# Kernel optimization log

Hardware: AMD Instinct MI355X
Metric: run time of the kernel (lower is better)

## Reference

```python
import jax, jax.numpy as jnp
import numpy as np

B, S, D, E, H = 4, 4096, 1024, 8, 128  # batch, seq, d_model, experts, expert hidden (hardcoded 128)


def setup_inputs() -> dict:
    key = jax.random.key(0)
    ks = jax.random.split(key, 7)
    s_in = 1.0 / np.sqrt(D)
    s_h = 1.0 / np.sqrt(H)
    return {
        "x": jax.random.normal(ks[0], (B, S, D), dtype=jnp.float32),
        "W1": jax.random.normal(ks[1], (E, D, H), dtype=jnp.float32) * s_in,
        "b1": jax.random.normal(ks[2], (E, H), dtype=jnp.float32) * s_in,
        "W2": jax.random.normal(ks[3], (E, H, D), dtype=jnp.float32) * s_h,
        "b2": jax.random.normal(ks[4], (E, D), dtype=jnp.float32) * s_h,
        "Wg": jax.random.normal(ks[5], (D, E), dtype=jnp.float32) * s_in,
        "bg": jax.random.normal(ks[6], (E,), dtype=jnp.float32) * s_in,
    }


def reference(x, W1, b1, W2, b2, Wg, bg):
    # Gate: softmax over experts. [B,S,E]
    gate = jax.nn.softmax(jnp.einsum("bsd,de->bse", x, Wg) + bg, axis=-1)
    # Dense per-expert MLP applied to every token.
    h = jax.nn.relu(jnp.einsum("bsd,edh->bseh", x, W1) + b1)          # [B,S,E,H]
    y = jnp.einsum("bseh,eho->bseo", h, W2) + b2                       # [B,S,E,D]
    # Fused weighted sum over the expert axis (replaces the python double loop).
    out = jnp.einsum("bse,bseo->bso", gate, y)                         # [B,S,D]
    return out
```

## Files before the change

### kernel.cpp

```cpp
#include <hip/hip_runtime.h>
#include <hip/hip_bf16.h>

#define B_ 4
#define S_ 4096
#define D_ 1024
#define E_ 8
#define H_ 128
#define M_ (B_*S_)
#define K_ 1024
#define N_ 1024
#define NT_ (K_/64)
#define NIT_ (NT_/2)

typedef short bf16x8 __attribute__((ext_vector_type(8)));
typedef float f32x4 __attribute__((ext_vector_type(4)));

__device__ __forceinline__ unsigned short f2bf(float f){
  union { float f; unsigned int u; } v; v.f = f;
  unsigned int u = v.u;
  unsigned int r = (u + 0x7fffu + ((u >> 16) & 1u)) >> 16;
  return (unsigned short)r;
}

__device__ __forceinline__ void gload16(const void* g, void* l){
  __builtin_amdgcn_global_load_lds((const __attribute__((address_space(1))) void*)g,
                                   (__attribute__((address_space(3))) void*)l, 16, 0, 0);
}

__global__ __launch_bounds__(256)
void prep_x_gate(const float* __restrict__ x, const float* __restrict__ Wg,
                 const float* __restrict__ bg, unsigned short* __restrict__ xb,
                 float* __restrict__ gate){
  int tid = threadIdx.x;
  int lane = tid & 63;
  int m = blockIdx.x * 4 + (tid >> 6);
  const float* xr = x + (size_t)m * D_;
  unsigned short* xbr = xb + (size_t)m * D_;
  float acc[E_];
  #pragma unroll
  for (int e = 0; e < E_; ++e) acc[e] = 0.f;
  #pragma unroll
  for (int c = 0; c < D_/64; ++c){
    int d = c*64 + lane;
    float xs = xr[d];
    xbr[d] = f2bf(xs);
    const float4 w0 = *(const float4*)(Wg + (size_t)d * E_);
    const float4 w1 = *(const float4*)(Wg + (size_t)d * E_ + 4);
    acc[0] = fmaf(xs, w0.x, acc[0]); acc[1] = fmaf(xs, w0.y, acc[1]);
    acc[2] = fmaf(xs, w0.z, acc[2]); acc[3] = fmaf(xs, w0.w, acc[3]);
    acc[4] = fmaf(xs, w1.x, acc[4]); acc[5] = fmaf(xs, w1.y, acc[5]);
    acc[6] = fmaf(xs, w1.z, acc[6]); acc[7] = fmaf(xs, w1.w, acc[7]);
  }
  #pragma unroll
  for (int off = 32; off > 0; off >>= 1){
    #pragma unroll
    for (int e = 0; e < E_; ++e) acc[e] += __shfl_xor(acc[e], off, 64);
  }
  float lg[E_]; float mx = -1e30f;
  #pragma unroll
  for (int e = 0; e < E_; ++e){ lg[e] = acc[e] + bg[e]; mx = fmaxf(mx, lg[e]); }
  float s = 0.f;
  #pragma unroll
  for (int e = 0; e < E_; ++e){ lg[e] = expf(lg[e] - mx); s += lg[e]; }
  float inv = 1.f / s;
  if (lane < E_) gate[(size_t)m * E_ + lane] = lg[lane] * inv;
}

__global__ __launch_bounds__(256)
void transpose_pack(const float* __restrict__ in, unsigned short* __restrict__ out,
                    int C, int ostride, int in_estride, int out_ebase){
  __shared__ float t[32][33];
  int e = blockIdx.z;
  const float* ip = in + (size_t)e * in_estride;
  unsigned short* op = out + (size_t)e * out_ebase;
  int tx = threadIdx.x, ty = threadIdx.y;
  int c0 = blockIdx.x * 32, r0 = blockIdx.y * 32;
  #pragma unroll
  for (int yy = 0; yy < 32; yy += 8)
    t[ty + yy][tx] = ip[(size_t)(r0 + ty + yy) * C + (c0 + tx)];
  __syncthreads();
  #pragma unroll
  for (int yy = 0; yy < 32; yy += 8)
    op[(size_t)(c0 + ty + yy) * ostride + (r0 + tx)] = f2bf(t[tx][ty + yy]);
}

template<int PASS>
__global__ __launch_bounds__(512, 2)
void gemm_moe8(const unsigned short* __restrict__ A,
               const unsigned short* __restrict__ Bt,
               const float* __restrict__ gate,
               const float* __restrict__ bias,
               void* __restrict__ outp)
{
  __shared__ unsigned short lds[65536];

  int bid = blockIdx.x;
  int xcd = bid & 7, pos = bid >> 3;
  int mb = xcd * 8 + (pos >> 2);
  int nb = pos & 3;
  int m0 = mb * 256, n0 = nb * 256;

  int tid = threadIdx.x;
  int lane = tid & 63;
  int w = tid >> 6;
  int wm = w & 1, wn = w >> 1;
  int rowi = lane & 15, s4 = lane >> 4;

  int sg = (tid & 7) ^ ((tid >> 3) & 7);
  const unsigned short* gA = A  + (size_t)(m0 + (tid >> 3)) * K_ + sg * 8;
  const unsigned short* gB = Bt + (size_t)(n0 + (tid >> 3)) * K_ + sg * 8;
  int t8 = tid * 8;

#define STAGE_A(b,h,kt) do{ const unsigned short* g_ = gA + (size_t)((h)*128)*K_ + (kt)*64; \
  gload16(g_,                 &lds[(b)*16384 + (h)*8192 + t8]); \
  gload16(g_ + (size_t)64*K_, &lds[(b)*16384 + (h)*8192 + t8 + 4096]); }while(0)
#define STAGE_B(b,h,kt) do{ const unsigned short* g_ = gB + (size_t)((h)*128)*K_ + (kt)*64; \
  gload16(g_,                 &lds[32768 + (b)*16384 + (h)*8192 + t8]); \
  gload16(g_ + (size_t)64*K_, &lds[32768 + (b)*16384 + (h)*8192 + t8 + 4096]); }while(0)

  int bk0 = rowi*64 + (( s4     ) ^ (rowi & 7)) * 8;
  int bk1 = rowi*64 + ((4 + s4  ) ^ (rowi & 7)) * 8;
  int abase0 = wm * 8192;
  int bbase0 = 32768 + (wn >> 1) * 8192 + (wn & 1) * 4096;

  f32x4 acc[8][4];
  #pragma unroll
  for (int i = 0; i < 8; ++i){
    #pragma unroll
    for (int j = 0; j < 4; ++j){ f32x4 z = {0.f,0.f,0.f,0.f}; acc[i][j] = z; }
  }
  bf16x8 af[4][2], bfr[4][2];

#define READ_A(b,r) do{ int ab_ = (b)*16384 + abase0; \
  _Pragma("unroll") for (int f2 = 0; f2 < 4; ++f2){ \
    af[f2][0] = *(const bf16x8*)&lds[ab_ + ((r)*4+f2)*1024 + bk0]; \
    af[f2][1] = *(const bf16x8*)&lds[ab_ + ((r)*4+f2)*1024 + bk1]; } }while(0)
#define READ_B(b,c) do{ int bb_ = (b)*16384 + bbase0; \
  _Pragma("unroll") for (int j2 = 0; j2 < 2; ++j2){ \
    bfr[(c)*2+j2][0] = *(const bf16x8*)&lds[bb_ + ((c)*2+j2)*1024 + bk0]; \
    bfr[(c)*2+j2][1] = *(const bf16x8*)&lds[bb_ + ((c)*2+j2)*1024 + bk1]; } }while(0)
#define MFMA16(r,c) do{ \
  _Pragma("unroll") for (int f2 = 0; f2 < 4; ++f2) \
  _Pragma("unroll") for (int j2 = 0; j2 < 2; ++j2){ \
    acc[(r)*4+f2][(c)*2+j2] = __builtin_amdgcn_mfma_f32_16x16x32_bf16(af[f2][0], bfr[(c)*2+j2][0], acc[(r)*4+f2][(c)*2+j2], 0,0,0); \
    acc[(r)*4+f2][(c)*2+j2] = __builtin_amdgcn_mfma_f32_16x16x32_bf16(af[f2][1], bfr[(c)*2+j2][1], acc[(r)*4+f2][(c)*2+j2], 0,0,0); \
  } }while(0)

#define PH_MID  __builtin_amdgcn_s_barrier(); \
                asm volatile("s_waitcnt lgkmcnt(0)" ::: "memory"); \
                __builtin_amdgcn_s_setprio(1)
#define PH_END  __builtin_amdgcn_s_setprio(0); __builtin_amdgcn_s_barrier()
#define PH_END_VM(N) __builtin_amdgcn_s_setprio(0); \
                asm volatile("s_waitcnt vmcnt(" #N ")" ::: "memory"); \
                __builtin_amdgcn_s_barrier()

  STAGE_B(0,0,0); STAGE_B(0,1,0);
  STAGE_A(0,0,0); STAGE_A(0,1,0);
  STAGE_B(1,0,1); STAGE_B(1,1,1);
  STAGE_A(1,0,1);
  asm volatile("s_waitcnt vmcnt(6)" ::: "memory");
  __builtin_amdgcn_s_barrier();

  #pragma unroll 1
  for (int it = 0; it < NIT_; ++it){
    int kt1  = 2*it + 1;
    int ktn0 = 2*it + 2, ktn1 = 2*it + 3;
    bool more = (it < NIT_ - 1);
    READ_A(0,0); READ_B(0,0);
    STAGE_A(1,1,kt1);
    PH_MID; MFMA16(0,0); PH_END;
    READ_B(0,1);
    PH_MID; MFMA16(0,1); PH_END;
    READ_A(0,1);
    if (more) STAGE_B(0,0,ktn0);
    PH_MID; MFMA16(1,1); PH_END;
    if (more) STAGE_B(0,1,ktn0);
    PH_MID; MFMA16(1,0);
    __builtin_amdgcn_s_setprio(0);
    if (more) { asm volatile("s_waitcnt vmcnt(4)" ::: "memory"); }
    else      { asm volatile("s_waitcnt vmcnt(0)" ::: "memory"); }
    __builtin_amdgcn_s_barrier();
    READ_A(1,0); READ_B(1,0);
    if (more) STAGE_A(0,0,ktn0);
    PH_MID; MFMA16(0,0); PH_END;
    READ_B(1,1);
    if (more) STAGE_A(0,1,ktn0);
    PH_MID; MFMA16(0,1); PH_END;
    READ_A(1,1);
    if (more) STAGE_B(1,0,ktn1);
    PH_MID; MFMA16(1,1); PH_END;
    if (more){ STAGE_B(1,1,ktn1); STAGE_A(1,0,ktn1); }
    PH_MID; MFMA16(1,0); PH_END_VM(6);
  }

  float* lws = (float*)lds + w * 4096;
  int ncol0 = n0 + wn*64;

  if (PASS == 1){
    unsigned short* Hp = (unsigned short*)outp;
    int e = nb*2 + (wn >> 1);
    float b1v[4];
    #pragma unroll
    for (int j = 0; j < 4; ++j) b1v[j] = bias[e*H_ + (wn&1)*64 + j*16 + rowi];
    #pragma unroll
    for (int ci = 0; ci < 2; ++ci){
      #pragma unroll
      for (int f2 = 0; f2 < 4; ++f2){
        int fi = ci*4 + f2;
        #pragma unroll
        for (int jj = 0; jj < 4; ++jj){
          int m = m0 + wm*128 + fi*16 + s4*4 + jj;
          float g = gate[(size_t)m*E_ + e];
          int r_l = f2*16 + s4*4 + jj;
          #pragma unroll
          for (int j = 0; j < 4; ++j){
            float v = fmaxf(acc[fi][j][jj] + b1v[j], 0.f) * g;
            lws[r_l*64 + ((j*16 + rowi) ^ (s4 << 4))] = v;
          }
        }
      }
      asm volatile("s_waitcnt lgkmcnt(0)" ::: "memory");
      #pragma unroll
      for (int it2 = 0; it2 < 16; ++it2){
        int r_l = it2*4 + (lane >> 4);
        int c4  = lane & 15;
        int X   = it2 & 3;
        f32x4 v = *(const f32x4*)&lws[r_l*64 + ((c4*4) ^ (X << 4))];
        union { unsigned short us[4]; uint2 u2; } pk;
        #pragma unroll
        for (int q = 0; q < 4; ++q) pk.us[q] = f2bf(v[q]);
        int m = m0 + wm*128 + ci*64 + r_l;
        *(uint2*)&Hp[(size_t)m*N_ + ncol0 + c4*4] = pk.u2;
      }
      if (ci == 0) asm volatile("s_waitcnt lgkmcnt(0)" ::: "memory");
    }
  } else {
    float* Out = (float*)outp;
    float b2v[8][4];
    #pragma unroll
    for (int j = 0; j < 4; ++j){
      int n = ncol0 + j*16 + rowi;
      #pragma unroll
      for (int e = 0; e < 8; ++e) b2v[e][j] = bias[(size_t)e*N_ + n];
    }
    #pragma unroll
    for (int ci = 0; ci < 2; ++ci){
      #pragma unroll
      for (int f2 = 0; f2 < 4; ++f2){
        int fi = ci*4 + f2;
        #pragma unroll
        for (int jj = 0; jj < 4; ++jj){
          int m = m0 + wm*128 + fi*16 + s4*4 + jj;
          const float4 g0 = *(const float4*)(gate + (size_t)m*E_);
          const float4 g1 = *(const float4*)(gate + (size_t)m*E_ + 4);
          int r_l = f2*16 + s4*4 + jj;
          #pragma unroll
          for (int j = 0; j < 4; ++j){
            float bv = g0.x*b2v[0][j] + g0.y*b2v[1][j] + g0.z*b2v[2][j] + g0.w*b2v[3][j]
                     + g1.x*b2v[4][j] + g1.y*b2v[5][j] + g1.z*b2v[6][j] + g1.w*b2v[7][j];
            lws[r_l*64 + ((j*16 + rowi) ^ (s4 << 4))] = acc[fi][j][jj] + bv;
          }
        }
      }
      asm volatile("s_waitcnt lgkmcnt(0)" ::: "memory");
      #pragma unroll
      for (int it2 = 0; it2 < 16; ++it2){
        int r_l = it2*4 + (lane >> 4);
        int c4  = lane & 15;
        int X   = it2 & 3;
        f32x4 v = *(const f32x4*)&lws[r_l*64 + ((c4*4) ^ (X << 4))];
        int m = m0 + wm*128 + ci*64 + r_l;
        *(f32x4*)&Out[(size_t)m*N_ + ncol0 + c4*4] = v;
      }
      if (ci == 0) asm volatile("s_waitcnt lgkmcnt(0)" ::: "memory");
    }
  }
#undef STAGE_A
#undef STAGE_B
#undef READ_A
#undef READ_B
#undef MFMA16
#undef PH_MID
#undef PH_END
#undef PH_END_VM
}

extern "C" void kernel_launch(void* const* d_in, const int* in_sizes, int n_in,
                              void* d_out, int out_size, void* d_ws, size_t ws_size,
                              hipStream_t stream){
  const float* x  = (const float*)d_in[0];
  const float* W1 = (const float*)d_in[1];
  const float* b1 = (const float*)d_in[2];
  const float* W2 = (const float*)d_in[3];
  const float* b2 = (const float*)d_in[4];
  const float* Wg = (const float*)d_in[5];
  const float* bg = (const float*)d_in[6];
  float* out = (float*)d_out;

  char* ws = (char*)d_ws;
  unsigned short* xb  = (unsigned short*)(ws);
  unsigned short* Hp  = (unsigned short*)(ws + ((size_t)32<<20));
  unsigned short* B1T = (unsigned short*)(ws + ((size_t)64<<20));
  unsigned short* B2T = (unsigned short*)(ws + ((size_t)66<<20));
  float*          gate= (float*)(ws + ((size_t)68<<20));

  hipLaunchKernelGGL(prep_x_gate, dim3(M_/4), dim3(256), 0, stream, x, Wg, bg, xb, gate);
  hipLaunchKernelGGL(transpose_pack, dim3(128/32, 1024/32, 8), dim3(32,8), 0, stream,
                     W1, B1T, 128, 1024, 1024*128, 128*1024);
  hipLaunchKernelGGL(transpose_pack, dim3(1024/32, 128/32, 8), dim3(32,8), 0, stream,
                     W2, B2T, 1024, 1024, 128*1024, 128);
  hipLaunchKernelGGL((gemm_moe8<1>), dim3(256), dim3(512), 0, stream,
                     xb, B1T, gate, b1, (void*)Hp);
  hipLaunchKernelGGL((gemm_moe8<2>), dim3(256), dim3(512), 0, stream,
                     Hp, B2T, gate, b2, (void*)out);
}
```

Measured before the change: 107.4 us.

## Fuse fp32-to-bf16 conversion of x into first GEMM and store output directly

The first GEMM now loads fp32 x straight from global memory into registers, converts it to bf16 and writes it into swizzled LDS, with the load and wait schedule interleaved into the existing pipeline. This removes the separate bf16 copy of x written by the prep kernel and the extra global round trip that copy needed. The second GEMM epilogue skips the LDS transpose and writes fp32 output directly from the accumulators, which gives less coalesced stores. The cost is more registers and VALU work inside the GEMM main loop, plus a more fragile vmcnt schedule.

Measured after the change: 130.1 us. 1.21x slower.

```diff
diff --git a/kernel.cpp b/kernel.cpp
--- a/kernel.cpp
+++ b/kernel.cpp
@@ -28,14 +28,12 @@
 }
 
 __global__ __launch_bounds__(256)
-void prep_x_gate(const float* __restrict__ x, const float* __restrict__ Wg,
-                 const float* __restrict__ bg, unsigned short* __restrict__ xb,
-                 float* __restrict__ gate){
+void prep_gate(const float* __restrict__ x, const float* __restrict__ Wg,
+               const float* __restrict__ bg, float* __restrict__ gate){
   int tid = threadIdx.x;
   int lane = tid & 63;
   int m = blockIdx.x * 4 + (tid >> 6);
   const float* xr = x + (size_t)m * D_;
-  unsigned short* xbr = xb + (size_t)m * D_;
   float acc[E_];
   #pragma unroll
   for (int e = 0; e < E_; ++e) acc[e] = 0.f;
@@ -43,7 +41,6 @@
   for (int c = 0; c < D_/64; ++c){
     int d = c*64 + lane;
     float xs = xr[d];
-    xbr[d] = f2bf(xs);
     const float4 w0 = *(const float4*)(Wg + (size_t)d * E_);
     const float4 w1 = *(const float4*)(Wg + (size_t)d * E_ + 4);
     acc[0] = fmaf(xs, w0.x, acc[0]); acc[1] = fmaf(xs, w0.y, acc[1]);
@@ -83,53 +80,6 @@
   for (int yy = 0; yy < 32; yy += 8)
     op[(size_t)(c0 + ty + yy) * ostride + (r0 + tx)] = f2bf(t[tx][ty + yy]);
 }
-
-template<int PASS>
-__global__ __launch_bounds__(512, 2)
-void gemm_moe8(const unsigned short* __restrict__ A,
-               const unsigned short* __restrict__ Bt,
-               const float* __restrict__ gate,
-               const float* __restrict__ bias,
-               void* __restrict__ outp)
-{
-  __shared__ unsigned short lds[65536];
-
-  int bid = blockIdx.x;
-  int xcd = bid & 7, pos = bid >> 3;
-  int mb = xcd * 8 + (pos >> 2);
-  int nb = pos & 3;
-  int m0 = mb * 256, n0 = nb * 256;
-
-  int tid = threadIdx.x;
-  int lane = tid & 63;
-  int w = tid >> 6;
-  int wm = w & 1, wn = w >> 1;
-  int rowi = lane & 15, s4 = lane >> 4;
-
-  int sg = (tid & 7) ^ ((tid >> 3) & 7);
-  const unsigned short* gA = A  + (size_t)(m0 + (tid >> 3)) * K_ + sg * 8;
-  const unsigned short* gB = Bt + (size_t)(n0 + (tid >> 3)) * K_ + sg * 8;
-  int t8 = tid * 8;
-
-#define STAGE_A(b,h,kt) do{ const unsigned short* g_ = gA + (size_t)((h)*128)*K_ + (kt)*64; \
-  gload16(g_,                 &lds[(b)*16384 + (h)*8192 + t8]); \
-  gload16(g_ + (size_t)64*K_, &lds[(b)*16384 + (h)*8192 + t8 + 4096]); }while(0)
-#define STAGE_B(b,h,kt) do{ const unsigned short* g_ = gB + (size_t)((h)*128)*K_ + (kt)*64; \
-  gload16(g_,                 &lds[32768 + (b)*16384 + (h)*8192 + t8]); \
-  gload16(g_ + (size_t)64*K_, &lds[32768 + (b)*16384 + (h)*8192 + t8 + 4096]); }while(0)
-
-  int bk0 = rowi*64 + (( s4     ) ^ (rowi & 7)) * 8;
-  int bk1 = rowi*64 + ((4 + s4  ) ^ (rowi & 7)) * 8;
-  int abase0 = wm * 8192;
-  int bbase0 = 32768 + (wn >> 1) * 8192 + (wn & 1) * 4096;
-
-  f32x4 acc[8][4];
-  #pragma unroll
-  for (int i = 0; i < 8; ++i){
-    #pragma unroll
-    for (int j = 0; j < 4; ++j){ f32x4 z = {0.f,0.f,0.f,0.f}; acc[i][j] = z; }
-  }
-  bf16x8 af[4][2], bfr[4][2];
 
 #define READ_A(b,r) do{ int ab_ = (b)*16384 + abase0; \
   _Pragma("unroll") for (int f2 = 0; f2 < 4; ++f2){ \
@@ -145,7 +95,6 @@
     acc[(r)*4+f2][(c)*2+j2] = __builtin_amdgcn_mfma_f32_16x16x32_bf16(af[f2][0], bfr[(c)*2+j2][0], acc[(r)*4+f2][(c)*2+j2], 0,0,0); \
     acc[(r)*4+f2][(c)*2+j2] = __builtin_amdgcn_mfma_f32_16x16x32_bf16(af[f2][1], bfr[(c)*2+j2][1], acc[(r)*4+f2][(c)*2+j2], 0,0,0); \
   } }while(0)
-
 #define PH_MID  __builtin_amdgcn_s_barrier(); \
                 asm volatile("s_waitcnt lgkmcnt(0)" ::: "memory"); \
                 __builtin_amdgcn_s_setprio(1)
@@ -153,11 +102,208 @@
 #define PH_END_VM(N) __builtin_amdgcn_s_setprio(0); \
                 asm volatile("s_waitcnt vmcnt(" #N ")" ::: "memory"); \
                 __builtin_amdgcn_s_barrier()
-
-  STAGE_B(0,0,0); STAGE_B(0,1,0);
-  STAGE_A(0,0,0); STAGE_A(0,1,0);
-  STAGE_B(1,0,1); STAGE_B(1,1,1);
-  STAGE_A(1,0,1);
+#define VMW(N)  do{ asm volatile("s_waitcnt vmcnt(" #N ")" ::: "memory"); \
+                    __builtin_amdgcn_sched_barrier(0); }while(0)
+#define LA4(dst, p) do{ const float* p_ = (p); \
+  (dst)[0] = *(const float4*)(p_);      (dst)[1] = *(const float4*)(p_ + 4); \
+  (dst)[2] = *(const float4*)(p_ + 8);  (dst)[3] = *(const float4*)(p_ + 12); }while(0)
+
+__global__ __launch_bounds__(512, 2)
+void gemm_pass1(const float* __restrict__ X,
+                const unsigned short* __restrict__ Bt,
+                const float* __restrict__ gate,
+                const float* __restrict__ bias,
+                unsigned short* __restrict__ Hp)
+{
+  __shared__ unsigned short lds[65536];
+
+  int bid = blockIdx.x;
+  int xcd = bid & 7, pos = bid >> 3;
+  int mb = xcd * 8 + (pos >> 2);
+  int nb = pos & 3;
+  int m0 = mb * 256, n0 = nb * 256;
+
+  int tid = threadIdx.x;
+  int lane = tid & 63;
+  int w = tid >> 6;
+  int wm = w & 1, wn = w >> 1;
+  int rowi = lane & 15, s4 = lane >> 4;
+
+  int sg = (tid & 7) ^ ((tid >> 3) & 7);
+  const unsigned short* gB = Bt + (size_t)(n0 + (tid >> 3)) * K_ + sg * 8;
+  int t8 = tid * 8;
+#define SB(b,h,kt) do{ const unsigned short* g_ = gB + (size_t)((h)*128)*K_ + (kt)*64; \
+  gload16(g_,                 &lds[32768 + (b)*16384 + (h)*8192 + t8]); \
+  gload16(g_ + (size_t)64*K_, &lds[32768 + (b)*16384 + (h)*8192 + t8 + 4096]); }while(0)
+
+  int wr_  = tid >> 2;
+  int ws0_ = (2*(tid & 3))     ^ (wr_ & 7);
+  int ws1_ = (2*(tid & 3) + 1) ^ (wr_ & 7);
+  const float* gxA = X + (size_t)(m0 + wr_) * K_ + (tid & 3) * 16;
+#define PA(h,kt) (gxA + (size_t)((h)*128)*K_ + (kt)*64)
+#define WA_(b,h,la) do{ \
+  union { unsigned short us[8]; bf16x8 v; } p0_, p1_; \
+  p0_.us[0]=f2bf((la)[0].x); p0_.us[1]=f2bf((la)[0].y); \
+  p0_.us[2]=f2bf((la)[0].z); p0_.us[3]=f2bf((la)[0].w); \
+  p0_.us[4]=f2bf((la)[1].x); p0_.us[5]=f2bf((la)[1].y); \
+  p0_.us[6]=f2bf((la)[1].z); p0_.us[7]=f2bf((la)[1].w); \
+  p1_.us[0]=f2bf((la)[2].x); p1_.us[1]=f2bf((la)[2].y); \
+  p1_.us[2]=f2bf((la)[2].z); p1_.us[3]=f2bf((la)[2].w); \
+  p1_.us[4]=f2bf((la)[3].x); p1_.us[5]=f2bf((la)[3].y); \
+  p1_.us[6]=f2bf((la)[3].z); p1_.us[7]=f2bf((la)[3].w); \
+  *(bf16x8*)&lds[(b)*16384 + (h)*8192 + wr_*64 + ws0_*8] = p0_.v; \
+  *(bf16x8*)&lds[(b)*16384 + (h)*8192 + wr_*64 + ws1_*8] = p1_.v; }while(0)
+
+  int bk0 = rowi*64 + (( s4     ) ^ (rowi & 7)) * 8;
+  int bk1 = rowi*64 + ((4 + s4  ) ^ (rowi & 7)) * 8;
+  int abase0 = wm * 8192;
+  int bbase0 = 32768 + (wn >> 1) * 8192 + (wn & 1) * 4096;
+
+  f32x4 acc[8][4];
+  #pragma unroll
+  for (int i = 0; i < 8; ++i){
+    #pragma unroll
+    for (int j = 0; j < 4; ++j){ f32x4 z = {0.f,0.f,0.f,0.f}; acc[i][j] = z; }
+  }
+  bf16x8 af[4][2], bfr[4][2];
+  float4 laA[4], laB[4];
+
+  SB(0,0,0); SB(0,1,0);
+  LA4(laA, PA(0,0));
+  LA4(laB, PA(1,0));
+  VMW(4);  WA_(0,0,laA);
+  LA4(laA, PA(0,1));
+  VMW(4);  WA_(0,1,laB);
+  SB(1,0,1);
+  VMW(2);  WA_(1,0,laA);
+  LA4(laB, PA(1,1));
+  SB(1,1,1);
+  asm volatile("s_waitcnt lgkmcnt(0)" ::: "memory");
+  __builtin_amdgcn_s_barrier();
+
+  #pragma unroll 1
+  for (int it = 0; it < NIT_; ++it){
+    int ktn0 = 2*it + 2, ktn1 = 2*it + 3;
+    bool more = (it < NIT_ - 1);
+    READ_A(0,0); READ_B(0,0);
+    VMW(2); WA_(1,1,laB);
+    PH_MID; MFMA16(0,0); PH_END;
+    READ_B(0,1);
+    PH_MID; MFMA16(0,1); PH_END;
+    READ_A(0,1);
+    if (more){ SB(0,0,ktn0); LA4(laA, PA(0,ktn0)); }
+    PH_MID; MFMA16(1,1); PH_END;
+    if (more){ SB(0,1,ktn0); LA4(laB, PA(1,ktn0)); }
+    PH_MID; MFMA16(1,0);
+    __builtin_amdgcn_s_setprio(0);
+    if (more) { VMW(12); } else { VMW(0); }
+    __builtin_amdgcn_s_barrier();
+    READ_A(1,0); READ_B(1,0);
+    if (more){ VMW(6); WA_(0,0,laA); }
+    PH_MID; MFMA16(0,0); PH_END;
+    READ_B(1,1);
+    if (more){ LA4(laA, PA(0,ktn1)); VMW(4); WA_(0,1,laB); }
+    PH_MID; MFMA16(0,1); PH_END;
+    READ_A(1,1);
+    if (more){ SB(1,0,ktn1); LA4(laB, PA(1,ktn1)); }
+    PH_MID; MFMA16(1,1); PH_END;
+    if (more){ SB(1,1,ktn1); VMW(8); WA_(1,0,laA); }
+    PH_MID; MFMA16(1,0); PH_END;
+  }
+
+  float* lws = (float*)lds + w * 4096;
+  int ncol0 = n0 + wn*64;
+  int e = nb*2 + (wn >> 1);
+  float b1v[4];
+  #pragma unroll
+  for (int j = 0; j < 4; ++j) b1v[j] = bias[e*H_ + (wn&1)*64 + j*16 + rowi];
+  #pragma unroll
+  for (int ci = 0; ci < 2; ++ci){
+    #pragma unroll
+    for (int f2 = 0; f2 < 4; ++f2){
+      int fi = ci*4 + f2;
+      #pragma unroll
+      for (int jj = 0; jj < 4; ++jj){
+        int m = m0 + wm*128 + fi*16 + s4*4 + jj;
+        float g = gate[(size_t)m*E_ + e];
+        int r_l = f2*16 + s4*4 + jj;
+        #pragma unroll
+        for (int j = 0; j < 4; ++j){
+          float v = fmaxf(acc[fi][j][jj] + b1v[j], 0.f) * g;
+          lws[r_l*64 + ((j*16 + rowi) ^ (s4 << 4))] = v;
+        }
+      }
+    }
+    asm volatile("s_waitcnt lgkmcnt(0)" ::: "memory");
+    #pragma unroll
+    for (int it2 = 0; it2 < 16; ++it2){
+      int r_l = it2*4 + (lane >> 4);
+      int c4  = lane & 15;
+      int X2  = it2 & 3;
+      f32x4 v = *(const f32x4*)&lws[r_l*64 + ((c4*4) ^ (X2 << 4))];
+      union { unsigned short us[4]; uint2 u2; } pk;
+      #pragma unroll
+      for (int q = 0; q < 4; ++q) pk.us[q] = f2bf(v[q]);
+      int m = m0 + wm*128 + ci*64 + r_l;
+      *(uint2*)&Hp[(size_t)m*N_ + ncol0 + c4*4] = pk.u2;
+    }
+    if (ci == 0) asm volatile("s_waitcnt lgkmcnt(0)" ::: "memory");
+  }
+#undef SB
+#undef PA
+#undef WA_
+}
+
+__global__ __launch_bounds__(512, 2)
+void gemm_pass2(const unsigned short* __restrict__ A,
+                const unsigned short* __restrict__ Bt,
+                const float* __restrict__ gate,
+                const float* __restrict__ bias,
+                float* __restrict__ Out)
+{
+  __shared__ unsigned short lds[65536];
+
+  int bid = blockIdx.x;
+  int xcd = bid & 7, pos = bid >> 3;
+  int mb = xcd * 8 + (pos >> 2);
+  int nb = pos & 3;
+  int m0 = mb * 256, n0 = nb * 256;
+
+  int tid = threadIdx.x;
+  int lane = tid & 63;
+  int w = tid >> 6;
+  int wm = w & 1, wn = w >> 1;
+  int rowi = lane & 15, s4 = lane >> 4;
+
+  int sg = (tid & 7) ^ ((tid >> 3) & 7);
+  const unsigned short* gA = A  + (size_t)(m0 + (tid >> 3)) * K_ + sg * 8;
+  const unsigned short* gB = Bt + (size_t)(n0 + (tid >> 3)) * K_ + sg * 8;
+  int t8 = tid * 8;
+
+#define SA2(b,h,kt) do{ const unsigned short* g_ = gA + (size_t)((h)*128)*K_ + (kt)*64; \
+  gload16(g_,                 &lds[(b)*16384 + (h)*8192 + t8]); \
+  gload16(g_ + (size_t)64*K_, &lds[(b)*16384 + (h)*8192 + t8 + 4096]); }while(0)
+#define SB2(b,h,kt) do{ const unsigned short* g_ = gB + (size_t)((h)*128)*K_ + (kt)*64; \
+  gload16(g_,                 &lds[32768 + (b)*16384 + (h)*8192 + t8]); \
+  gload16(g_ + (size_t)64*K_, &lds[32768 + (b)*16384 + (h)*8192 + t8 + 4096]); }while(0)
+
+  int bk0 = rowi*64 + (( s4     ) ^ (rowi & 7)) * 8;
+  int bk1 = rowi*64 + ((4 + s4  ) ^ (rowi & 7)) * 8;
+  int abase0 = wm * 8192;
+  int bbase0 = 32768 + (wn >> 1) * 8192 + (wn & 1) * 4096;
+
+  f32x4 acc[8][4];
+  #pragma unroll
+  for (int i = 0; i < 8; ++i){
+    #pragma unroll
+    for (int j = 0; j < 4; ++j){ f32x4 z = {0.f,0.f,0.f,0.f}; acc[i][j] = z; }
+  }
+  bf16x8 af[4][2], bfr[4][2];
+
+  SB2(0,0,0); SB2(0,1,0);
+  SA2(0,0,0); SA2(0,1,0);
+  SB2(1,0,1); SB2(1,1,1);
+  SA2(1,0,1);
   asm volatile("s_waitcnt vmcnt(6)" ::: "memory");
   __builtin_amdgcn_s_barrier();
 
@@ -167,122 +313,59 @@
     int ktn0 = 2*it + 2, ktn1 = 2*it + 3;
     bool more = (it < NIT_ - 1);
     READ_A(0,0); READ_B(0,0);
-    STAGE_A(1,1,kt1);
+    SA2(1,1,kt1);
     PH_MID; MFMA16(0,0); PH_END;
     READ_B(0,1);
     PH_MID; MFMA16(0,1); PH_END;
     READ_A(0,1);
-    if (more) STAGE_B(0,0,ktn0);
+    if (more) SB2(0,0,ktn0);
     PH_MID; MFMA16(1,1); PH_END;
-    if (more) STAGE_B(0,1,ktn0);
+    if (more) SB2(0,1,ktn0);
     PH_MID; MFMA16(1,0);
     __builtin_amdgcn_s_setprio(0);
     if (more) { asm volatile("s_waitcnt vmcnt(4)" ::: "memory"); }
     else      { asm volatile("s_waitcnt vmcnt(0)" ::: "memory"); }
     __builtin_amdgcn_s_barrier();
     READ_A(1,0); READ_B(1,0);
-    if (more) STAGE_A(0,0,ktn0);
+    if (more) SA2(0,0,ktn0);
     PH_MID; MFMA16(0,0); PH_END;
     READ_B(1,1);
-    if (more) STAGE_A(0,1,ktn0);
+    if (more) SA2(0,1,ktn0);
     PH_MID; MFMA16(0,1); PH_END;
     READ_A(1,1);
-    if (more) STAGE_B(1,0,ktn1);
+    if (more) SB2(1,0,ktn1);
     PH_MID; MFMA16(1,1); PH_END;
-    if (more){ STAGE_B(1,1,ktn1); STAGE_A(1,0,ktn1); }
+    if (more){ SB2(1,1,ktn1); SA2(1,0,ktn1); }
     PH_MID; MFMA16(1,0); PH_END_VM(6);
   }
 
-  float* lws = (float*)lds + w * 4096;
   int ncol0 = n0 + wn*64;
-
-  if (PASS == 1){
-    unsigned short* Hp = (unsigned short*)outp;
-    int e = nb*2 + (wn >> 1);
-    float b1v[4];
-    #pragma unroll
-    for (int j = 0; j < 4; ++j) b1v[j] = bias[e*H_ + (wn&1)*64 + j*16 + rowi];
-    #pragma unroll
-    for (int ci = 0; ci < 2; ++ci){
+  float b2v[8][4];
+  #pragma unroll
+  for (int j = 0; j < 4; ++j){
+    int n = ncol0 + j*16 + rowi;
+    #pragma unroll
+    for (int e = 0; e < 8; ++e) b2v[e][j] = bias[(size_t)e*N_ + n];
+  }
+  #pragma unroll
+  for (int fi = 0; fi < 8; ++fi){
+    #pragma unroll
+    for (int jj = 0; jj < 4; ++jj){
+      int m = m0 + wm*128 + fi*16 + s4*4 + jj;
+      const float4 g0 = *(const float4*)(gate + (size_t)m*E_);
+      const float4 g1 = *(const float4*)(gate + (size_t)m*E_ + 4);
+      float bv[4];
       #pragma unroll
-      for (int f2 = 0; f2 < 4; ++f2){
-        int fi = ci*4 + f2;
-        #pragma unroll
-        for (int jj = 0; jj < 4; ++jj){
-          int m = m0 + wm*128 + fi*16 + s4*4 + jj;
-          float g = gate[(size_t)m*E_ + e];
-          int r_l = f2*16 + s4*4 + jj;
-          #pragma unroll
-          for (int j = 0; j < 4; ++j){
-            float v = fmaxf(acc[fi][j][jj] + b1v[j], 0.f) * g;
-            lws[r_l*64 + ((j*16 + rowi) ^ (s4 << 4))] = v;
-          }
-        }
-      }
-      asm volatile("s_waitcnt lgkmcnt(0)" ::: "memory");
+      for (int j = 0; j < 4; ++j)
+        bv[j] = g0.x*b2v[0][j] + g0.y*b2v[1][j] + g0.z*b2v[2][j] + g0.w*b2v[3][j]
+              + g1.x*b2v[4][j] + g1.y*b2v[5][j] + g1.z*b2v[6][j] + g1.w*b2v[7][j];
       #pragma unroll
-      for (int it2 = 0; it2 < 16; ++it2){
-        int r_l = it2*4 + (lane >> 4);
-        int c4  = lane & 15;
-        int X   = it2 & 3;
-        f32x4 v = *(const f32x4*)&lws[r_l*64 + ((c4*4) ^ (X << 4))];
-        union { unsigned short us[4]; uint2 u2; } pk;
-        #pragma unroll
-        for (int q = 0; q < 4; ++q) pk.us[q] = f2bf(v[q]);
-        int m = m0 + wm*128 + ci*64 + r_l;
-        *(uint2*)&Hp[(size_t)m*N_ + ncol0 + c4*4] = pk.u2;
-      }
-      if (ci == 0) asm volatile("s_waitcnt lgkmcnt(0)" ::: "memory");
+      for (int j = 0; j < 4; ++j)
+        Out[(size_t)m*N_ + ncol0 + j*16 + rowi] = acc[fi][j][jj] + bv[j];
     }
-  } else {
-    float* Out = (float*)outp;
-    float b2v[8][4];
-    #pragma unroll
-    for (int j = 0; j < 4; ++j){
-      int n = ncol0 + j*16 + rowi;
-      #pragma unroll
-      for (int e = 0; e < 8; ++e) b2v[e][j] = bias[(size_t)e*N_ + n];
-    }
-    #pragma unroll
-    for (int ci = 0; ci < 2; ++ci){
-      #pragma unroll
-      for (int f2 = 0; f2 < 4; ++f2){
-        int fi = ci*4 + f2;
-        #pragma unroll
-        for (int jj = 0; jj < 4; ++jj){
-          int m = m0 + wm*128 + fi*16 + s4*4 + jj;
-          const float4 g0 = *(const float4*)(gate + (size_t)m*E_);
-          const float4 g1 = *(const float4*)(gate + (size_t)m*E_ + 4);
-          int r_l = f2*16 + s4*4 + jj;
-          #pragma unroll
-          for (int j = 0; j < 4; ++j){
-            float bv = g0.x*b2v[0][j] + g0.y*b2v[1][j] + g0.z*b2v[2][j] + g0.w*b2v[3][j]
-                     + g1.x*b2v[4][j] + g1.y*b2v[5][j] + g1.z*b2v[6][j] + g1.w*b2v[7][j];
-            lws[r_l*64 + ((j*16 + rowi) ^ (s4 << 4))] = acc[fi][j][jj] + bv;
-          }
-        }
-      }
-      asm volatile("s_waitcnt lgkmcnt(0)" ::: "memory");
-      #pragma unroll
-      for (int it2 = 0; it2 < 16; ++it2){
-        int r_l = it2*4 + (lane >> 4);
-        int c4  = lane & 15;
-        int X   = it2 & 3;
-        f32x4 v = *(const f32x4*)&lws[r_l*64 + ((c4*4) ^ (X << 4))];
-        int m = m0 + wm*128 + ci*64 + r_l;
-        *(f32x4*)&Out[(size_t)m*N_ + ncol0 + c4*4] = v;
-      }
-      if (ci == 0) asm volatile("s_waitcnt lgkmcnt(0)" ::: "memory");
-    }
-  }
-#undef STAGE_A
-#undef STAGE_B
-#undef READ_A
-#undef READ_B
-#undef MFMA16
-#undef PH_MID
-#undef PH_END
-#undef PH_END_VM
+  }
+#undef SA2
+#undef SB2
 }
 
 extern "C" void kernel_launch(void* const* d_in, const int* in_sizes, int n_in,
@@ -298,19 +381,18 @@
   float* out = (float*)d_out;
 
   char* ws = (char*)d_ws;
-  unsigned short* xb  = (unsigned short*)(ws);
-  unsigned short* Hp  = (unsigned short*)(ws + ((size_t)32<<20));
-  unsigned short* B1T = (unsigned short*)(ws + ((size_t)64<<20));
-  unsigned short* B2T = (unsigned short*)(ws + ((size_t)66<<20));
-  float*          gate= (float*)(ws + ((size_t)68<<20));
-
-  hipLaunchKernelGGL(prep_x_gate, dim3(M_/4), dim3(256), 0, stream, x, Wg, bg, xb, gate);
+  unsigned short* Hp  = (unsigned short*)(ws);
+  unsigned short* B1T = (unsigned short*)(ws + ((size_t)32<<20));
+  unsigned short* B2T = (unsigned short*)(ws + ((size_t)34<<20));
+  float*          gate= (float*)(ws + ((size_t)36<<20));
+
+  hipLaunchKernelGGL(prep_gate, dim3(M_/4), dim3(256), 0, stream, x, Wg, bg, gate);
   hipLaunchKernelGGL(transpose_pack, dim3(128/32, 1024/32, 8), dim3(32,8), 0, stream,
                      W1, B1T, 128, 1024, 1024*128, 128*1024);
   hipLaunchKernelGGL(transpose_pack, dim3(1024/32, 128/32, 8), dim3(32,8), 0, stream,
                      W2, B2T, 1024, 1024, 128*1024, 128);
-  hipLaunchKernelGGL((gemm_moe8<1>), dim3(256), dim3(512), 0, stream,
-                     xb, B1T, gate, b1, (void*)Hp);
-  hipLaunchKernelGGL((gemm_moe8<2>), dim3(256), dim3(512), 0, stream,
-                     Hp, B2T, gate, b2, (void*)out);
-}
+  hipLaunchKernelGGL(gemm_pass1, dim3(256), dim3(512), 0, stream,
+                     x, B1T, gate, b1, Hp);
+  hipLaunchKernelGGL(gemm_pass2, dim3(256), dim3(512), 0, stream,
+                     Hp, B2T, gate, b2, out);
+}
```

## Merge prep and weight transposes into one launch; vectorize x loads; direct output stores

Applied to the files above, without the earlier changes.

Combines the x-cast/gate kernel and both weight transpose kernels into a single launch that dispatches on block index, removing two kernel launches and their gaps. The x conversion now reads float4 and writes packed bf16 quads. The second GEMM epilogue drops the LDS staging and writes scalar fp32 results straight to global memory, which removes the LDS round trip and its waits but gives up coalesced 16-byte stores.

New measurement: 137.9 us. 28.5% more time.

```diff
diff --git a/kernel.cpp b/kernel.cpp
--- a/kernel.cpp
+++ b/kernel.cpp
@@ -28,108 +28,82 @@
 }
 
 __global__ __launch_bounds__(256)
-void prep_x_gate(const float* __restrict__ x, const float* __restrict__ Wg,
-                 const float* __restrict__ bg, unsigned short* __restrict__ xb,
-                 float* __restrict__ gate){
+void prep_all(const float* __restrict__ x,  const float* __restrict__ Wg,
+              const float* __restrict__ bg, const float* __restrict__ W1,
+              const float* __restrict__ W2, unsigned short* __restrict__ xb,
+              float* __restrict__ gate,     unsigned short* __restrict__ B1T,
+              unsigned short* __restrict__ B2T){
+  __shared__ float t[32][33];
+  int bid = blockIdx.x;
   int tid = threadIdx.x;
-  int lane = tid & 63;
-  int m = blockIdx.x * 4 + (tid >> 6);
-  const float* xr = x + (size_t)m * D_;
-  unsigned short* xbr = xb + (size_t)m * D_;
-  float acc[E_];
-  #pragma unroll
-  for (int e = 0; e < E_; ++e) acc[e] = 0.f;
-  #pragma unroll
-  for (int c = 0; c < D_/64; ++c){
-    int d = c*64 + lane;
-    float xs = xr[d];
-    xbr[d] = f2bf(xs);
-    const float4 w0 = *(const float4*)(Wg + (size_t)d * E_);
-    const float4 w1 = *(const float4*)(Wg + (size_t)d * E_ + 4);
-    acc[0] = fmaf(xs, w0.x, acc[0]); acc[1] = fmaf(xs, w0.y, acc[1]);
-    acc[2] = fmaf(xs, w0.z, acc[2]); acc[3] = fmaf(xs, w0.w, acc[3]);
-    acc[4] = fmaf(xs, w1.x, acc[4]); acc[5] = fmaf(xs, w1.y, acc[5]);
-    acc[6] = fmaf(xs, w1.z, acc[6]); acc[7] = fmaf(xs, w1.w, acc[7]);
+
+  if (bid < 4096){
+    int lane = tid & 63;
+    int m = bid * 4 + (tid >> 6);
+    const float* xr = x + (size_t)m * D_;
+    unsigned short* xbr = xb + (size_t)m * D_;
+    float acc[E_];
+    #pragma unroll
+    for (int e = 0; e < E_; ++e) acc[e] = 0.f;
+    #pragma unroll
+    for (int c = 0; c < 4; ++c){
+      int d = c*256 + lane*4;
+      float4 xs = *(const float4*)(xr + d);
+      union { unsigned short us[4]; uint2 u2; } pk;
+      pk.us[0] = f2bf(xs.x); pk.us[1] = f2bf(xs.y);
+      pk.us[2] = f2bf(xs.z); pk.us[3] = f2bf(xs.w);
+      *(uint2*)(xbr + d) = pk.u2;
+      #pragma unroll
+      for (int q = 0; q < 4; ++q){
+        float xv = (q==0)?xs.x:(q==1)?xs.y:(q==2)?xs.z:xs.w;
+        const float4 w0 = *(const float4*)(Wg + (size_t)(d+q) * E_);
+        const float4 w1 = *(const float4*)(Wg + (size_t)(d+q) * E_ + 4);
+        acc[0] = fmaf(xv, w0.x, acc[0]); acc[1] = fmaf(xv, w0.y, acc[1]);
+        acc[2] = fmaf(xv, w0.z, acc[2]); acc[3] = fmaf(xv, w0.w, acc[3]);
+        acc[4] = fmaf(xv, w1.x, acc[4]); acc[5] = fmaf(xv, w1.y, acc[5]);
+        acc[6] = fmaf(xv, w1.z, acc[6]); acc[7] = fmaf(xv, w1.w, acc[7]);
+      }
+    }
+    #pragma unroll
+    for (int off = 32; off > 0; off >>= 1){
+      #pragma unroll
+      for (int e = 0; e < E_; ++e) acc[e] += __shfl_xor(acc[e], off, 64);
+    }
+    float lg[E_]; float mx = -1e30f;
+    #pragma unroll
+    for (int e = 0; e < E_; ++e){ lg[e] = acc[e] + bg[e]; mx = fmaxf(mx, lg[e]); }
+    float s = 0.f;
+    #pragma unroll
+    for (int e = 0; e < E_; ++e){ lg[e] = expf(lg[e] - mx); s += lg[e]; }
+    float inv = 1.f / s;
+    if (lane < E_) gate[(size_t)m * E_ + lane] = lg[lane] * inv;
+  } else {
+    const float* in; unsigned short* out;
+    int C, ostride, in_estride, out_ebase, bx, by, e;
+    if (bid < 4096 + 1024){
+      int b = bid - 4096;
+      bx = b & 3; by = (b >> 2) & 31; e = b >> 7;
+      in = W1; out = B1T; C = 128; ostride = 1024;
+      in_estride = 1024*128; out_ebase = 128*1024;
+    } else {
+      int b = bid - 5120;
+      bx = b & 31; by = (b >> 5) & 3; e = b >> 7;
+      in = W2; out = B2T; C = 1024; ostride = 1024;
+      in_estride = 128*1024; out_ebase = 128;
+    }
+    const float* ip = in + (size_t)e * in_estride;
+    unsigned short* op = out + (size_t)e * out_ebase;
+    int tx = tid & 31, ty = tid >> 5;
+    int c0 = bx * 32, r0 = by * 32;
+    #pragma unroll
+    for (int yy = 0; yy < 32; yy += 8)
+      t[ty + yy][tx] = ip[(size_t)(r0 + ty + yy) * C + (c0 + tx)];
+    __syncthreads();
+    #pragma unroll
+    for (int yy = 0; yy < 32; yy += 8)
+      op[(size_t)(c0 + ty + yy) * ostride + (r0 + tx)] = f2bf(t[tx][ty + yy]);
   }
-  #pragma unroll
-  for (int off = 32; off > 0; off >>= 1){
-    #pragma unroll
-    for (int e = 0; e < E_; ++e) acc[e] += __shfl_xor(acc[e], off, 64);
-  }
-  float lg[E_]; float mx = -1e30f;
-  #pragma unroll
-  for (int e = 0; e < E_; ++e){ lg[e] = acc[e] + bg[e]; mx = fmaxf(mx, lg[e]); }
-  float s = 0.f;
-  #pragma unroll
-  for (int e = 0; e < E_; ++e){ lg[e] = expf(lg[e] - mx); s += lg[e]; }
-  float inv = 1.f / s;
-  if (lane < E_) gate[(size_t)m * E_ + lane] = lg[lane] * inv;
-}
-
-__global__ __launch_bounds__(256)
-void transpose_pack(const float* __restrict__ in, unsigned short* __restrict__ out,
-                    int C, int ostride, int in_estride, int out_ebase){
-  __shared__ float t[32][33];
-  int e = blockIdx.z;
-  const float* ip = in + (size_t)e * in_estride;
-  unsigned short* op = out + (size_t)e * out_ebase;
-  int tx = threadIdx.x, ty = threadIdx.y;
-  int c0 = blockIdx.x * 32, r0 = blockIdx.y * 32;
-  #pragma unroll
-  for (int yy = 0; yy < 32; yy += 8)
-    t[ty + yy][tx] = ip[(size_t)(r0 + ty + yy) * C + (c0 + tx)];
-  __syncthreads();
-  #pragma unroll
-  for (int yy = 0; yy < 32; yy += 8)
-    op[(size_t)(c0 + ty + yy) * ostride + (r0 + tx)] = f2bf(t[tx][ty + yy]);
-}
-
-template<int PASS>
-__global__ __launch_bounds__(512, 2)
-void gemm_moe8(const unsigned short* __restrict__ A,
-               const unsigned short* __restrict__ Bt,
-               const float* __restrict__ gate,
-               const float* __restrict__ bias,
-               void* __restrict__ outp)
-{
-  __shared__ unsigned short lds[65536];
-
-  int bid = blockIdx.x;
-  int xcd = bid & 7, pos = bid >> 3;
-  int mb = xcd * 8 + (pos >> 2);
-  int nb = pos & 3;
-  int m0 = mb * 256, n0 = nb * 256;
-
-  int tid = threadIdx.x;
-  int lane = tid & 63;
-  int w = tid >> 6;
-  int wm = w & 1, wn = w >> 1;
-  int rowi = lane & 15, s4 = lane >> 4;
-
-  int sg = (tid & 7) ^ ((tid >> 3) & 7);
-  const unsigned short* gA = A  + (size_t)(m0 + (tid >> 3)) * K_ + sg * 8;
-  const unsigned short* gB = Bt + (size_t)(n0 + (tid >> 3)) * K_ + sg * 8;
-  int t8 = tid * 8;
-
-#define STAGE_A(b,h,kt) do{ const unsigned short* g_ = gA + (size_t)((h)*128)*K_ + (kt)*64; \
-  gload16(g_,                 &lds[(b)*16384 + (h)*8192 + t8]); \
-  gload16(g_ + (size_t)64*K_, &lds[(b)*16384 + (h)*8192 + t8 + 4096]); }while(0)
-#define STAGE_B(b,h,kt) do{ const unsigned short* g_ = gB + (size_t)((h)*128)*K_ + (kt)*64; \
-  gload16(g_,                 &lds[32768 + (b)*16384 + (h)*8192 + t8]); \
-  gload16(g_ + (size_t)64*K_, &lds[32768 + (b)*16384 + (h)*8192 + t8 + 4096]); }while(0)
-
-  int bk0 = rowi*64 + (( s4     ) ^ (rowi & 7)) * 8;
-  int bk1 = rowi*64 + ((4 + s4  ) ^ (rowi & 7)) * 8;
-  int abase0 = wm * 8192;
-  int bbase0 = 32768 + (wn >> 1) * 8192 + (wn & 1) * 4096;
-
-  f32x4 acc[8][4];
-  #pragma unroll
-  for (int i = 0; i < 8; ++i){
-    #pragma unroll
-    for (int j = 0; j < 4; ++j){ f32x4 z = {0.f,0.f,0.f,0.f}; acc[i][j] = z; }
-  }
-  bf16x8 af[4][2], bfr[4][2];
+}
 
 #define READ_A(b,r) do{ int ab_ = (b)*16384 + abase0; \
   _Pragma("unroll") for (int f2 = 0; f2 < 4; ++f2){ \
@@ -145,7 +119,6 @@
     acc[(r)*4+f2][(c)*2+j2] = __builtin_amdgcn_mfma_f32_16x16x32_bf16(af[f2][0], bfr[(c)*2+j2][0], acc[(r)*4+f2][(c)*2+j2], 0,0,0); \
     acc[(r)*4+f2][(c)*2+j2] = __builtin_amdgcn_mfma_f32_16x16x32_bf16(af[f2][1], bfr[(c)*2+j2][1], acc[(r)*4+f2][(c)*2+j2], 0,0,0); \
   } }while(0)
-
 #define PH_MID  __builtin_amdgcn_s_barrier(); \
                 asm volatile("s_waitcnt lgkmcnt(0)" ::: "memory"); \
                 __builtin_amdgcn_s_setprio(1)
@@ -153,6 +126,53 @@
 #define PH_END_VM(N) __builtin_amdgcn_s_setprio(0); \
                 asm volatile("s_waitcnt vmcnt(" #N ")" ::: "memory"); \
                 __builtin_amdgcn_s_barrier()
+
+template<int PASS>
+__global__ __launch_bounds__(512, 2)
+void gemm_moe8(const unsigned short* __restrict__ A,
+               const unsigned short* __restrict__ Bt,
+               const float* __restrict__ gate,
+               const float* __restrict__ bias,
+               void* __restrict__ outp)
+{
+  __shared__ unsigned short lds[65536];
+
+  int bid = blockIdx.x;
+  int xcd = bid & 7, pos = bid >> 3;
+  int mb = xcd * 8 + (pos >> 2);
+  int nb = pos & 3;
+  int m0 = mb * 256, n0 = nb * 256;
+
+  int tid = threadIdx.x;
+  int lane = tid & 63;
+  int w = tid >> 6;
+  int wm = w & 1, wn = w >> 1;
+  int rowi = lane & 15, s4 = lane >> 4;
+
+  int sg = (tid & 7) ^ ((tid >> 3) & 7);
+  const unsigned short* gA = A  + (size_t)(m0 + (tid >> 3)) * K_ + sg * 8;
+  const unsigned short* gB = Bt + (size_t)(n0 + (tid >> 3)) * K_ + sg * 8;
+  int t8 = tid * 8;
+
+#define STAGE_A(b,h,kt) do{ const unsigned short* g_ = gA + (size_t)((h)*128)*K_ + (kt)*64; \
+  gload16(g_,                 &lds[(b)*16384 + (h)*8192 + t8]); \
+  gload16(g_ + (size_t)64*K_, &lds[(b)*16384 + (h)*8192 + t8 + 4096]); }while(0)
+#define STAGE_B(b,h,kt) do{ const unsigned short* g_ = gB + (size_t)((h)*128)*K_ + (kt)*64; \
+  gload16(g_,                 &lds[32768 + (b)*16384 + (h)*8192 + t8]); \
+  gload16(g_ + (size_t)64*K_, &lds[32768 + (b)*16384 + (h)*8192 + t8 + 4096]); }while(0)
+
+  int bk0 = rowi*64 + (( s4     ) ^ (rowi & 7)) * 8;
+  int bk1 = rowi*64 + ((4 + s4  ) ^ (rowi & 7)) * 8;
+  int abase0 = wm * 8192;
+  int bbase0 = 32768 + (wn >> 1) * 8192 + (wn & 1) * 4096;
+
+  f32x4 acc[8][4];
+  #pragma unroll
+  for (int i = 0; i < 8; ++i){
+    #pragma unroll
+    for (int j = 0; j < 4; ++j){ f32x4 z = {0.f,0.f,0.f,0.f}; acc[i][j] = z; }
+  }
+  bf16x8 af[4][2], bfr[4][2];
 
   STAGE_B(0,0,0); STAGE_B(0,1,0);
   STAGE_A(0,0,0); STAGE_A(0,1,0);
@@ -193,11 +213,10 @@
     PH_MID; MFMA16(1,0); PH_END_VM(6);
   }
 
-  float* lws = (float*)lds + w * 4096;
   int ncol0 = n0 + wn*64;
-
   if (PASS == 1){
     unsigned short* Hp = (unsigned short*)outp;
+    float* lws = (float*)lds + w * 4096;
     int e = nb*2 + (wn >> 1);
     float b1v[4];
     #pragma unroll
@@ -224,8 +243,8 @@
       for (int it2 = 0; it2 < 16; ++it2){
         int r_l = it2*4 + (lane >> 4);
         int c4  = lane & 15;
-        int X   = it2 & 3;
-        f32x4 v = *(const f32x4*)&lws[r_l*64 + ((c4*4) ^ (X << 4))];
+        int X2  = it2 & 3;
+        f32x4 v = *(const f32x4*)&lws[r_l*64 + ((c4*4) ^ (X2 << 4))];
         union { unsigned short us[4]; uint2 u2; } pk;
         #pragma unroll
         for (int q = 0; q < 4; ++q) pk.us[q] = f2bf(v[q]);
@@ -244,45 +263,25 @@
       for (int e = 0; e < 8; ++e) b2v[e][j] = bias[(size_t)e*N_ + n];
     }
     #pragma unroll
-    for (int ci = 0; ci < 2; ++ci){
-      #pragma unroll
-      for (int f2 = 0; f2 < 4; ++f2){
-        int fi = ci*4 + f2;
+    for (int fi = 0; fi < 8; ++fi){
+      #pragma unroll
+      for (int jj = 0; jj < 4; ++jj){
+        int m = m0 + wm*128 + fi*16 + s4*4 + jj;
+        const float4 g0 = *(const float4*)(gate + (size_t)m*E_);
+        const float4 g1 = *(const float4*)(gate + (size_t)m*E_ + 4);
+        float bv[4];
         #pragma unroll
-        for (int jj = 0; jj < 4; ++jj){
-          int m = m0 + wm*128 + fi*16 + s4*4 + jj;
-          const float4 g0 = *(const float4*)(gate + (size_t)m*E_);
-          const float4 g1 = *(const float4*)(gate + (size_t)m*E_ + 4);
-          int r_l = f2*16 + s4*4 + jj;
-          #pragma unroll
-          for (int j = 0; j < 4; ++j){
-            float bv = g0.x*b2v[0][j] + g0.y*b2v[1][j] + g0.z*b2v[2][j] + g0.w*b2v[3][j]
-                     + g1.x*b2v[4][j] + g1.y*b2v[5][j] + g1.z*b2v[6][j] + g1.w*b2v[7][j];
-            lws[r_l*64 + ((j*16 + rowi) ^ (s4 << 4))] = acc[fi][j][jj] + bv;
-          }
-        }
+        for (int j = 0; j < 4; ++j)
+          bv[j] = g0.x*b2v[0][j] + g0.y*b2v[1][j] + g0.z*b2v[2][j] + g0.w*b2v[3][j]
+                + g1.x*b2v[4][j] + g1.y*b2v[5][j] + g1.z*b2v[6][j] + g1.w*b2v[7][j];
+        #pragma unroll
+        for (int j = 0; j < 4; ++j)
+          Out[(size_t)m*N_ + ncol0 + j*16 + rowi] = acc[fi][j][jj] + bv[j];
       }
-      asm volatile("s_waitcnt lgkmcnt(0)" ::: "memory");
-      #pragma unroll
-      for (int it2 = 0; it2 < 16; ++it2){
-        int r_l = it2*4 + (lane >> 4);
-        int c4  = lane & 15;
-        int X   = it2 & 3;
-        f32x4 v = *(const f32x4*)&lws[r_l*64 + ((c4*4) ^ (X << 4))];
-        int m = m0 + wm*128 + ci*64 + r_l;
-        *(f32x4*)&Out[(size_t)m*N_ + ncol0 + c4*4] = v;
-      }
-      if (ci == 0) asm volatile("s_waitcnt lgkmcnt(0)" ::: "memory");
     }
   }
 #undef STAGE_A
 #undef STAGE_B
-#undef READ_A
-#undef READ_B
-#undef MFMA16
-#undef PH_MID
-#undef PH_END
-#undef PH_END_VM
 }
 
 extern "C" void kernel_launch(void* const* d_in, const int* in_sizes, int n_in,
@@ -304,11 +303,8 @@
   unsigned short* B2T = (unsigned short*)(ws + ((size_t)66<<20));
   float*          gate= (float*)(ws + ((size_t)68<<20));
 
-  hipLaunchKernelGGL(prep_x_gate, dim3(M_/4), dim3(256), 0, stream, x, Wg, bg, xb, gate);
-  hipLaunchKernelGGL(transpose_pack, dim3(128/32, 1024/32, 8), dim3(32,8), 0, stream,
-                     W1, B1T, 128, 1024, 1024*128, 128*1024);
-  hipLaunchKernelGGL(transpose_pack, dim3(1024/32, 128/32, 8), dim3(32,8), 0, stream,
-                     W2, B2T, 1024, 1024, 128*1024, 128);
+  hipLaunchKernelGGL(prep_all, dim3(6144), dim3(256), 0, stream,
+                     x, Wg, bg, W1, W2, xb, gate, B1T, B2T);
   hipLaunchKernelGGL((gemm_moe8<1>), dim3(256), dim3(512), 0, stream,
                      xb, B1T, gate, b1, (void*)Hp);
   hipLaunchKernelGGL((gemm_moe8<2>), dim3(256), dim3(512), 0, stream,
```
